# Optimization experiments

Hardware: AMD Instinct MI355X
Metric: run time of the kernel (lower is better)

## Reference

```python
import jax, jax.numpy as jnp
import numpy as np

BS, TPD, D = 16384, 4, 128
G, M = 4, 4096


def setup_inputs() -> dict:
    key = jax.random.key(0)
    k1, k2 = jax.random.split(key)
    return {
        "x": jax.random.normal(k1, (BS, TPD, D), dtype=jnp.float32),
        "embeddings": jax.random.normal(k2, (G, M, D), dtype=jnp.float32),
        "count": jnp.zeros((G, M), dtype=jnp.float32),
    }


def reference(x, embeddings, count):
    bs, tpd, d = x.shape
    g, m, _ = embeddings.shape
    # (BS, TPD, D) -> (N, G, D) -> (G, N, D), N = BS*TPD/G
    xg = x.reshape(-1, g, d).transpose(1, 0, 2)
    # squared euclidean distances (argmin identical to cdist argmin)
    x2 = jnp.sum(xg * xg, axis=-1)[:, :, None]            # (G, N, 1)
    e2 = jnp.sum(embeddings * embeddings, axis=-1)[:, None, :]  # (G, 1, M)
    dist = x2 + e2 - 2.0 * jnp.einsum('gnd,gmd->gnm', xg, embeddings)  # (G, N, M)
    indices = jnp.argmin(dist, axis=-1)                   # (G, N) int
    # usage-count scatter add (buffer update in torch forward)
    new_count = count.at[jnp.arange(g)[:, None], indices].add(1.0)
    # gather quantized embeddings: (G, N, D)
    x_quant = embeddings[jnp.arange(g)[:, None], indices]
    x_quant = x_quant.transpose(1, 0, 2).reshape(bs, tpd, d)
    ind_out = indices.transpose(1, 0).reshape(bs, tpd)
    return (x_quant, ind_out, new_count)
```

## Files before the change

kernel.cpp:

```cpp
#include <hip/hip_runtime.h>

#define G 4
#define M 4096
#define D 128
#define NQ 16384
#define NROWS 65536
#define OFF_IND 8388608
#define OFF_CNT (OFF_IND + NROWS)
#define DELTA 0.02f

typedef unsigned int u32;
typedef unsigned short u16;
typedef __attribute__((ext_vector_type(8))) short bf16x8;
typedef __attribute__((ext_vector_type(4))) float f32x4;
typedef __attribute__((ext_vector_type(16))) float f32x16;

__device__ __forceinline__ u16 f2bf(float f) {
    u32 u = __float_as_uint(f);
    return (u16)((u + 0x7FFFu + ((u >> 16) & 1u)) >> 16);
}
__device__ __forceinline__ float bf2f(u16 b) { return __uint_as_float((u32)b << 16); }

union bfpack { bf16x8 v; u32 u[4]; };


__global__ __launch_bounds__(256) void e2both(const float* __restrict__ emb,
                                              float* __restrict__ e2f,
                                              double* __restrict__ e2d,
                                              int* __restrict__ flagcnt) {
    const int row = blockIdx.x * 4 + (threadIdx.x >> 6);
    const int lane = threadIdx.x & 63;
    const float2 v = ((const float2*)(emb + (size_t)row * D))[lane];
    double s = (double)v.x * (double)v.x + (double)v.y * (double)v.y;
#pragma unroll
    for (int off = 1; off < 64; off <<= 1) s += __shfl_xor(s, off, 64);
    if (lane == 0) { e2f[row] = (float)s; e2d[row] = s; }
    if (blockIdx.x == 0 && threadIdx.x == 0) *flagcnt = 0;
}

__global__ __launch_bounds__(256) void prep_emb(const float* __restrict__ emb,
                                                u32* __restrict__ efrag) {
    const int tid = threadIdx.x;
    const int g = blockIdx.x >> 7, mt = blockIdx.x & 127;
    u32* chunk = efrag + (size_t)(g * 128 + mt) * 4096;
#pragma unroll
    for (int rep = 0; rep < 2; ++rep) {
        const int idx = rep * 256 + tid;
        const int kk = idx >> 6, lane = idx & 63;
        const int m = mt * 32 + (lane & 31);
        const int k = kk * 16 + (lane >> 5) * 8;
        const float* src = emb + ((size_t)g * M + m) * D + k;
        const float4 a = *(const float4*)src;
        const float4 b = *(const float4*)(src + 4);
        const float v[8] = {a.x, a.y, a.z, a.w, b.x, b.y, b.z, b.w};
        u32 hi[4], lo[4];
#pragma unroll
        for (int i = 0; i < 4; ++i) {
            const float v0 = v[2 * i], v1 = v[2 * i + 1];
            const u16 h0 = f2bf(v0), h1 = f2bf(v1);
            const u16 l0 = f2bf(v0 - bf2f(h0)), l1 = f2bf(v1 - bf2f(h1));
            hi[i] = (u32)h0 | ((u32)h1 << 16);
            lo[i] = (u32)l0 | ((u32)l1 << 16);
        }
        *(uint4*)(chunk + (size_t)((kk * 2 + 0) * 64 + lane) * 4) = make_uint4(hi[0], hi[1], hi[2], hi[3]);
        *(uint4*)(chunk + (size_t)((kk * 2 + 1) * 64 + lane) * 4) = make_uint4(lo[0], lo[1], lo[2], lo[3]);
    }
}

__global__ __launch_bounds__(256, 3) void vq_mfma3(const float* __restrict__ x,
                                                   const u32* __restrict__ efrag,
                                                   const float* __restrict__ e2f,
                                                   float* __restrict__ pb1,
                                                   float* __restrict__ pb2,
                                                   int* __restrict__ pi1) {
    __shared__ float e2s[2048];
    __shared__ u32 ebuf[2][4096];

    const int tid = threadIdx.x, w = tid >> 6, lane = tid & 63;
    const int combo = blockIdx.x & 7;
    const int g = combo >> 1, half = combo & 1;
    const int qb = blockIdx.x >> 3;

    const float* e2g = e2f + (size_t)g * M + half * 2048;
    for (int i = tid; i < 512; i += 256) ((float4*)e2s)[i] = ((const float4*)e2g)[i];

    const int qrow = qb * 128 + w * 32 + (lane & 31);
    bf16x8 xh[8], xl[8];
#pragma unroll
    for (int kk = 0; kk < 8; ++kk) {
        const int k = kk * 16 + (lane >> 5) * 8;
        const float* src = x + ((size_t)qrow * 4 + g) * D + k;
        const float4 a = *(const float4*)src;
        const float4 b = *(const float4*)(src + 4);
        const float v[8] = {a.x, a.y, a.z, a.w, b.x, b.y, b.z, b.w};
        bfpack ph, pl;
#pragma unroll
        for (int i = 0; i < 4; ++i) {
            const float v0 = -2.0f * v[2 * i], v1 = -2.0f * v[2 * i + 1];
            const u16 h0 = f2bf(v0), h1 = f2bf(v1);
            const u16 l0 = f2bf(v0 - bf2f(h0)), l1 = f2bf(v1 - bf2f(h1));
            ph.u[i] = (u32)h0 | ((u32)h1 << 16);
            pl.u[i] = (u32)l0 | ((u32)l1 << 16);
        }
        xh[kk] = ph.v;
        xl[kk] = pl.v;
    }

    float b1[16], b2[16];
    int i1[16];
#pragma unroll
    for (int r = 0; r < 16; ++r) { b1[r] = 3.4e38f; b2[r] = 3.4e38f; i1[r] = 0; }

    const uint4* eg = (const uint4*)(efrag + (size_t)(g * 128 + half * 64) * 4096);
    {
        const uint4 t0 = eg[tid], t1 = eg[256 + tid], t2 = eg[512 + tid], t3 = eg[768 + tid];
        uint4* db = (uint4*)ebuf[0];
        db[tid] = t0; db[256 + tid] = t1; db[512 + tid] = t2; db[768 + tid] = t3;
    }
    __syncthreads();

    for (int t = 0; t < 64; ++t) {
        const int cur = t & 1;
        uint4 s0, s1, s2, s3;
        if (t < 63) {
            const uint4* src = eg + (size_t)(t + 1) * 1024;
            s0 = src[tid]; s1 = src[256 + tid]; s2 = src[512 + tid]; s3 = src[768 + tid];
        }
        const bf16x8* bp = (const bf16x8*)ebuf[cur];
        const float e2c = e2s[t * 32 + (lane & 31)];
        f32x16 acc;
#pragma unroll
        for (int r = 0; r < 16; ++r) acc[r] = e2c;
        __builtin_amdgcn_s_setprio(1);
#pragma unroll
        for (int kk = 0; kk < 8; ++kk) {
            const bf16x8 bh = bp[(kk * 2 + 0) * 64 + lane];
            const bf16x8 bl = bp[(kk * 2 + 1) * 64 + lane];
            acc = __builtin_amdgcn_mfma_f32_32x32x16_bf16(xl[kk], bh, acc, 0, 0, 0);
            acc = __builtin_amdgcn_mfma_f32_32x32x16_bf16(xh[kk], bl, acc, 0, 0, 0);
            acc = __builtin_amdgcn_mfma_f32_32x32x16_bf16(xh[kk], bh, acc, 0, 0, 0);
        }
        __builtin_amdgcn_s_setprio(0);
        const int mcol = half * 2048 + t * 32 + (lane & 31);
#pragma unroll
        for (int r = 0; r < 16; ++r) {
            const float s = acc[r];
            b2[r] = __builtin_amdgcn_fmed3f(s, b1[r], b2[r]);
            i1[r] = (s < b1[r]) ? mcol : i1[r];
            b1[r] = fminf(b1[r], s);
        }
        if (t < 63) {
            uint4* db = (uint4*)ebuf[cur ^ 1];
            db[tid] = s0; db[256 + tid] = s1; db[512 + tid] = s2; db[768 + tid] = s3;
        }
        __syncthreads();
    }

#pragma unroll
    for (int r = 0; r < 16; ++r) {
        float v1 = b1[r], v2 = b2[r];
        int j1 = i1[r];
#pragma unroll
        for (int off = 1; off < 32; off <<= 1) {
            const float o1 = __shfl_xor(v1, off, 64);
            const int   oj = __shfl_xor(j1, off, 64);
            const float o2 = __shfl_xor(v2, off, 64);
            v2 = fminf(fminf(v2, o2), fmaxf(v1, o1));
            if (o1 < v1 || (o1 == v1 && oj < j1)) { v1 = o1; j1 = oj; }
        }
        if ((lane & 31) == 0) {
            const int q = qb * 128 + w * 32 + (r & 3) + 8 * (r >> 2) + 4 * (lane >> 5);
            const int pidx = ((((g << 14) | q)) << 1) | half;
            pb1[pidx] = v1;
            pb2[pidx] = v2;
            pi1[pidx] = j1;
        }
    }
}

__global__ __launch_bounds__(256) void merge_kernel(const float* __restrict__ pb1,
                                                    const float* __restrict__ pb2,
                                                    const int* __restrict__ pi1,
                                                    float* __restrict__ out,
                                                    int* __restrict__ flagcnt,
                                                    int* __restrict__ flaglist) {
    const int t = blockIdx.x * 256 + threadIdx.x;
    const float v1a = pb1[2 * t], v1b = pb1[2 * t + 1];
    const float v2a = pb2[2 * t], v2b = pb2[2 * t + 1];
    const int   ia = pi1[2 * t],  ib = pi1[2 * t + 1];
    const float v1 = fminf(v1a, v1b);
    const int   i  = (v1b < v1a) ? ib : ia;
    const float v2 = fminf(fminf(v2a, v2b), fmaxf(v1a, v1b));
    const int g = t >> 14, n = t & 16383;
    if (v2 - v1 > DELTA) {
        out[(size_t)OFF_IND + (size_t)n * 4 + g] = (float)i;
        atomicAdd(out + OFF_CNT + (size_t)g * M + i, 1.0f);
    } else {
        const int pos = atomicAdd(flagcnt, 1);
        flaglist[pos] = t;
    }
}

__global__ __launch_bounds__(256) void recheck(const float* __restrict__ x,
                                               const float* __restrict__ emb,
                                               const double* __restrict__ e2d,
                                               const int* __restrict__ flagcnt,
                                               const int* __restrict__ flaglist,
                                               float* __restrict__ out) {
    __shared__ float xs[D];
    __shared__ double wv[4];
    __shared__ int wi[4];
    const int tid = threadIdx.x;
    int nf = *flagcnt;
    if (nf > NROWS) nf = NROWS;
    for (int it = blockIdx.x; it < nf; it += gridDim.x) {
        const int qid = flaglist[it];
        const int g = qid >> 14, n = qid & 16383;
        __syncthreads();
        if (tid < 32) ((float4*)xs)[tid] = ((const float4*)(x + ((size_t)n * 4 + g) * D))[tid];
        __syncthreads();
        double best = 1e300;
        int bi = 0;
        for (int j = 0; j < 16; ++j) {
            const int m = tid + j * 256;
            const float* e = emb + ((size_t)g * M + m) * D;
            double dot = 0.0;
            for (int k = 0; k < D; k += 4) {
                const float4 ev = *(const float4*)(e + k);
                dot = fma((double)xs[k + 0], (double)ev.x, dot);
                dot = fma((double)xs[k + 1], (double)ev.y, dot);
                dot = fma((double)xs[k + 2], (double)ev.z, dot);
                dot = fma((double)xs[k + 3], (double)ev.w, dot);
            }
            const double s = e2d[(size_t)g * M + m] - 2.0 * dot;
            if (s < best) { best = s; bi = m; }
        }
        for (int off = 1; off < 64; off <<= 1) {
            const double ob = __shfl_xor(best, off, 64);
            const int oi = __shfl_xor(bi, off, 64);
            if (ob < best || (ob == best && oi < bi)) { best = ob; bi = oi; }
        }
        if ((tid & 63) == 0) { wv[tid >> 6] = best; wi[tid >> 6] = bi; }
        __syncthreads();
        if (tid == 0) {
            double bv = wv[0];
            int bj = wi[0];
            for (int u = 1; u < 4; ++u)
                if (wv[u] < bv || (wv[u] == bv && wi[u] < bj)) { bv = wv[u]; bj = wi[u]; }
            out[(size_t)OFF_IND + (size_t)n * 4 + g] = (float)bj;
            atomicAdd(out + OFF_CNT + (size_t)g * M + bj, 1.0f);
        }
    }
}

__global__ __launch_bounds__(256) void gather_kernel(const float* __restrict__ emb,
                                                     const float* __restrict__ indf,
                                                     float* __restrict__ xq) {
    const int rid = blockIdx.x * 8 + (threadIdx.x >> 5);
    const int lane = threadIdx.x & 31;
    const int g = rid & 3;
    const int m = (int)indf[rid];
    const float4 v = ((const float4*)(emb + ((size_t)g * M + m) * D))[lane];
    ((float4*)(xq + (size_t)rid * D))[lane] = v;
}


#define QT 64
#define MT 128
#define KT 32
#define XPAD 132
#define EPAD 36

__global__ __launch_bounds__(256) void e2d_kernel(const float* __restrict__ emb,
                                                  double* __restrict__ e2) {
    int row = blockIdx.x * 4 + (threadIdx.x >> 6);
    int lane = threadIdx.x & 63;
    const float2 v = ((const float2*)(emb + (size_t)row * D))[lane];
    double s = (double)v.x * (double)v.x + (double)v.y * (double)v.y;
#pragma unroll
    for (int off = 1; off < 64; off <<= 1) s += __shfl_xor(s, off, 64);
    if (lane == 0) e2[row] = s;
}

__global__ __launch_bounds__(256) void argmin_kernel(const float* __restrict__ x,
                                                     const float* __restrict__ emb,
                                                     const double* __restrict__ e2,
                                                     float* __restrict__ out) {
    __shared__ float xs[QT][XPAD];
    __shared__ float es[MT][EPAD];
    const int g = blockIdx.x >> 8;
    const int n0 = (blockIdx.x & 255) * QT;
    const int tid = threadIdx.x;
    const int tm = tid & 15;
    const int tq = tid >> 4;
#pragma unroll
    for (int it = 0; it < 8; ++it) {
        int idx = it * 256 + tid;
        int r = idx >> 5, c2 = idx & 31;
        const float4 v = ((const float4*)(x + ((size_t)((n0 + r) * 4 + g)) * D))[c2];
        *(float4*)&xs[r][c2 * 4] = v;
    }
    double best[4];
    int bm[4];
#pragma unroll
    for (int qi = 0; qi < 4; ++qi) { best[qi] = 1e300; bm[qi] = 0; }
    const double* e2g = e2 + (size_t)g * M;
    const float* eg = emb + (size_t)g * M * D;
    for (int mc = 0; mc < M / MT; ++mc) {
        const int m0 = mc * MT;
        double acc[4][8];
#pragma unroll
        for (int qi = 0; qi < 4; ++qi)
#pragma unroll
            for (int mi = 0; mi < 8; ++mi) acc[qi][mi] = 0.0;
        for (int kc = 0; kc < D / KT; ++kc) {
            __syncthreads();
#pragma unroll
            for (int it = 0; it < 4; ++it) {
                int idx = it * 256 + tid;
                int r = idx >> 3, c2 = idx & 7;
                const float4 v = ((const float4*)(eg + (size_t)(m0 + r) * D + kc * KT))[c2];
                *(float4*)&es[r][c2 * 4] = v;
            }
            __syncthreads();
#pragma unroll
            for (int kk = 0; kk < KT; kk += 4) {
                double xv[4][4];
#pragma unroll
                for (int qi = 0; qi < 4; ++qi) {
                    const float4 v = *(const float4*)&xs[tq + 16 * qi][kc * KT + kk];
                    xv[qi][0] = v.x; xv[qi][1] = v.y; xv[qi][2] = v.z; xv[qi][3] = v.w;
                }
#pragma unroll
                for (int mi = 0; mi < 8; ++mi) {
                    const float4 v = *(const float4*)&es[tm + 16 * mi][kk];
                    const double e0 = v.x, e1 = v.y, e2v = v.z, e3 = v.w;
#pragma unroll
                    for (int qi = 0; qi < 4; ++qi) {
                        acc[qi][mi] = fma(xv[qi][0], e0, acc[qi][mi]);
                        acc[qi][mi] = fma(xv[qi][1], e1, acc[qi][mi]);
                        acc[qi][mi] = fma(xv[qi][2], e2v, acc[qi][mi]);
                        acc[qi][mi] = fma(xv[qi][3], e3, acc[qi][mi]);
                    }
                }
            }
        }
#pragma unroll
        for (int mi = 0; mi < 8; ++mi) {
            const int m = m0 + tm + 16 * mi;
            const double e2m = e2g[m];
#pragma unroll
            for (int qi = 0; qi < 4; ++qi) {
                const double s = e2m - 2.0 * acc[qi][mi];
                if (s < best[qi]) { best[qi] = s; bm[qi] = m; }
            }
        }
    }
#pragma unroll
    for (int qi = 0; qi < 4; ++qi) {
        double v = best[qi];
        int i = bm[qi];
#pragma unroll
        for (int off = 1; off < 16; off <<= 1) {
            const double ov = __shfl_xor(v, off, 64);
            const int oi = __shfl_xor(i, off, 64);
            if (ov < v || (ov == v && oi < i)) { v = ov; i = oi; }
        }
        if (tm == 0) {
            const int n = n0 + tq + 16 * qi;
            out[(size_t)OFF_IND + (size_t)n * 4 + g] = (float)i;
            atomicAdd(out + OFF_CNT + (size_t)g * M + i, 1.0f);
        }
    }
}


extern "C" void kernel_launch(void* const* d_in, const int* in_sizes, int n_in,
                              void* d_out, int out_size, void* d_ws, size_t ws_size,
                              hipStream_t stream) {
    const float* x   = (const float*)d_in[0];
    const float* emb = (const float*)d_in[1];
    const float* cnt = (const float*)d_in[2];
    float* out = (float*)d_out;

    if (ws_size >= 8454148) {
        u32*    efrag   = (u32*)d_ws;
        float*  e2fp    = (float*)((char*)d_ws + 8388608);
        int*    flagcnt = (int*)((char*)d_ws + 8454144);
        float*  pb1      = out;
        float*  pb2      = out + 131072;
        int*    pi1      = (int*)(out + 262144);
        int*    flaglist = (int*)(out + 393216);
        double* e2d      = (double*)(out + 458752);

        hipLaunchKernelGGL(e2both, dim3(4096), dim3(256), 0, stream, emb, e2fp, e2d, flagcnt);
        hipLaunchKernelGGL(prep_emb, dim3(512), dim3(256), 0, stream, emb, efrag);
        hipMemcpyAsync(out + OFF_CNT, cnt, (size_t)G * M * sizeof(float),
                       hipMemcpyDeviceToDevice, stream);
        hipLaunchKernelGGL(vq_mfma3, dim3(1024), dim3(256), 0, stream,
                           x, efrag, e2fp, pb1, pb2, pi1);
        hipLaunchKernelGGL(merge_kernel, dim3(256), dim3(256), 0, stream,
                           pb1, pb2, pi1, out, flagcnt, flaglist);
        hipLaunchKernelGGL(recheck, dim3(2048), dim3(256), 0, stream,
                           x, emb, e2d, flagcnt, flaglist, out);
        hipLaunchKernelGGL(gather_kernel, dim3(NROWS / 8), dim3(256), 0, stream,
                           emb, out + OFF_IND, out);
    } else {
        double* e2 = (double*)d_ws;
        hipLaunchKernelGGL(e2d_kernel, dim3(4096), dim3(256), 0, stream, emb, e2);
        hipMemcpyAsync(out + OFF_CNT, cnt, (size_t)G * M * sizeof(float),
                       hipMemcpyDeviceToDevice, stream);
        hipLaunchKernelGGL(argmin_kernel, dim3((NQ / QT) * G), dim3(256), 0, stream,
                           x, emb, e2, out);
        hipLaunchKernelGGL(gather_kernel, dim3(NROWS / 8), dim3(256), 0, stream,
                           emb, out + OFF_IND, out);
    }
}
```

Baseline: 375.2 us.

## Fuse prep kernels, use direct LDS loads, merge gather into argmin merge

```diff
diff --git a/kernel.cpp b/kernel.cpp
--- a/kernel.cpp
+++ b/kernel.cpp
@@ -23,26 +23,23 @@
 
 union bfpack { bf16x8 v; u32 u[4]; };
 
-
-__global__ __launch_bounds__(256) void e2both(const float* __restrict__ emb,
-                                              float* __restrict__ e2f,
-                                              double* __restrict__ e2d,
-                                              int* __restrict__ flagcnt) {
-    const int row = blockIdx.x * 4 + (threadIdx.x >> 6);
-    const int lane = threadIdx.x & 63;
-    const float2 v = ((const float2*)(emb + (size_t)row * D))[lane];
-    double s = (double)v.x * (double)v.x + (double)v.y * (double)v.y;
-#pragma unroll
-    for (int off = 1; off < 64; off <<= 1) s += __shfl_xor(s, off, 64);
-    if (lane == 0) { e2f[row] = (float)s; e2d[row] = s; }
-    if (blockIdx.x == 0 && threadIdx.x == 0) *flagcnt = 0;
-}
-
-__global__ __launch_bounds__(256) void prep_emb(const float* __restrict__ emb,
-                                                u32* __restrict__ efrag) {
-    const int tid = threadIdx.x;
+__device__ __forceinline__ void gload16(const void* gsrc, void* ldsdst) {
+    __builtin_amdgcn_global_load_lds(
+        (const __attribute__((address_space(1))) u32*)gsrc,
+        (__attribute__((address_space(3))) u32*)ldsdst,
+        16, 0, 0);
+}
+
+
+__global__ __launch_bounds__(256) void prep_all(const float* __restrict__ emb,
+                                                u32* __restrict__ efrag,
+                                                float* __restrict__ e2f,
+                                                int* __restrict__ flagcnt) {
+    __shared__ float part[4][32];
+    const int tid = threadIdx.x, w = tid >> 6;
     const int g = blockIdx.x >> 7, mt = blockIdx.x & 127;
     u32* chunk = efrag + (size_t)(g * 128 + mt) * 4096;
+    float ss = 0.f;
 #pragma unroll
     for (int rep = 0; rep < 2; ++rep) {
         const int idx = rep * 256 + tid;
@@ -53,6 +50,8 @@
         const float4 a = *(const float4*)src;
         const float4 b = *(const float4*)(src + 4);
         const float v[8] = {a.x, a.y, a.z, a.w, b.x, b.y, b.z, b.w};
+#pragma unroll
+        for (int i = 0; i < 8; ++i) ss = fmaf(v[i], v[i], ss);
         u32 hi[4], lo[4];
 #pragma unroll
         for (int i = 0; i < 4; ++i) {
@@ -65,14 +64,18 @@
         *(uint4*)(chunk + (size_t)((kk * 2 + 0) * 64 + lane) * 4) = make_uint4(hi[0], hi[1], hi[2], hi[3]);
         *(uint4*)(chunk + (size_t)((kk * 2 + 1) * 64 + lane) * 4) = make_uint4(lo[0], lo[1], lo[2], lo[3]);
     }
-}
-
-__global__ __launch_bounds__(256, 3) void vq_mfma3(const float* __restrict__ x,
+    ss += __shfl_xor(ss, 32, 64);
+    if ((tid & 63) < 32) part[w][tid & 31] = ss;
+    __syncthreads();
+    if (tid < 32)
+        e2f[(size_t)g * M + mt * 32 + tid] = part[0][tid] + part[1][tid] + part[2][tid] + part[3][tid];
+    if (blockIdx.x == 0 && tid == 0) *flagcnt = 0;
+}
+
+__global__ __launch_bounds__(256, 3) void vq_mfma4(const float* __restrict__ x,
                                                    const u32* __restrict__ efrag,
                                                    const float* __restrict__ e2f,
-                                                   float* __restrict__ pb1,
-                                                   float* __restrict__ pb2,
-                                                   int* __restrict__ pi1) {
+                                                   float* __restrict__ out) {
     __shared__ float e2s[2048];
     __shared__ u32 ebuf[2][4096];
 
@@ -111,27 +114,27 @@
 #pragma unroll
     for (int r = 0; r < 16; ++r) { b1[r] = 3.4e38f; b2[r] = 3.4e38f; i1[r] = 0; }
 
-    const uint4* eg = (const uint4*)(efrag + (size_t)(g * 128 + half * 64) * 4096);
-    {
-        const uint4 t0 = eg[tid], t1 = eg[256 + tid], t2 = eg[512 + tid], t3 = eg[768 + tid];
-        uint4* db = (uint4*)ebuf[0];
-        db[tid] = t0; db[256 + tid] = t1; db[512 + tid] = t2; db[768 + tid] = t3;
-    }
+    const char* eg = (const char*)(efrag + (size_t)(g * 128 + half * 64) * 4096);
+#pragma unroll
+    for (int j = 0; j < 4; ++j)
+        gload16(eg + j * 4096 + w * 1024 + lane * 16,
+                (char*)ebuf[0] + j * 4096 + w * 1024);
     __syncthreads();
 
+    int cur = 0;
     for (int t = 0; t < 64; ++t) {
-        const int cur = t & 1;
-        uint4 s0, s1, s2, s3;
         if (t < 63) {
-            const uint4* src = eg + (size_t)(t + 1) * 1024;
-            s0 = src[tid]; s1 = src[256 + tid]; s2 = src[512 + tid]; s3 = src[768 + tid];
+            const char* src = eg + (size_t)(t + 1) * 16384;
+#pragma unroll
+            for (int j = 0; j < 4; ++j)
+                gload16(src + j * 4096 + w * 1024 + lane * 16,
+                        (char*)ebuf[cur ^ 1] + j * 4096 + w * 1024);
         }
         const bf16x8* bp = (const bf16x8*)ebuf[cur];
         const float e2c = e2s[t * 32 + (lane & 31)];
         f32x16 acc;
 #pragma unroll
         for (int r = 0; r < 16; ++r) acc[r] = e2c;
-        __builtin_amdgcn_s_setprio(1);
 #pragma unroll
         for (int kk = 0; kk < 8; ++kk) {
             const bf16x8 bh = bp[(kk * 2 + 0) * 64 + lane];
@@ -140,7 +143,6 @@
             acc = __builtin_amdgcn_mfma_f32_32x32x16_bf16(xh[kk], bl, acc, 0, 0, 0);
             acc = __builtin_amdgcn_mfma_f32_32x32x16_bf16(xh[kk], bh, acc, 0, 0, 0);
         }
-        __builtin_amdgcn_s_setprio(0);
         const int mcol = half * 2048 + t * 32 + (lane & 31);
 #pragma unroll
         for (int r = 0; r < 16; ++r) {
@@ -149,11 +151,8 @@
             i1[r] = (s < b1[r]) ? mcol : i1[r];
             b1[r] = fminf(b1[r], s);
         }
-        if (t < 63) {
-            uint4* db = (uint4*)ebuf[cur ^ 1];
-            db[tid] = s0; db[256 + tid] = s1; db[512 + tid] = s2; db[768 + tid] = s3;
-        }
         __syncthreads();
+        cur ^= 1;
     }
 
 #pragma unroll
@@ -170,46 +169,63 @@
         }
         if ((lane & 31) == 0) {
             const int q = qb * 128 + w * 32 + (r & 3) + 8 * (r >> 2) + 4 * (lane >> 5);
-            const int pidx = ((((g << 14) | q)) << 1) | half;
-            pb1[pidx] = v1;
-            pb2[pidx] = v2;
-            pi1[pidx] = j1;
-        }
-    }
-}
-
-__global__ __launch_bounds__(256) void merge_kernel(const float* __restrict__ pb1,
-                                                    const float* __restrict__ pb2,
-                                                    const int* __restrict__ pi1,
+            float* rowbase = out + (size_t)(q * 4 + g) * D;
+            *(float4*)(rowbase + half * 4) =
+                make_float4(v1, v2, __int_as_float(j1), 0.f);
+        }
+    }
+}
+
+__global__ __launch_bounds__(256) void gather_merge(const float* __restrict__ emb,
                                                     float* __restrict__ out,
                                                     int* __restrict__ flagcnt,
                                                     int* __restrict__ flaglist) {
-    const int t = blockIdx.x * 256 + threadIdx.x;
-    const float v1a = pb1[2 * t], v1b = pb1[2 * t + 1];
-    const float v2a = pb2[2 * t], v2b = pb2[2 * t + 1];
-    const int   ia = pi1[2 * t],  ib = pi1[2 * t + 1];
-    const float v1 = fminf(v1a, v1b);
-    const int   i  = (v1b < v1a) ? ib : ia;
-    const float v2 = fminf(fminf(v2a, v2b), fmaxf(v1a, v1b));
-    const int g = t >> 14, n = t & 16383;
-    if (v2 - v1 > DELTA) {
+    __shared__ int sm[64];
+    const int tid = threadIdx.x;
+    const int qid0 = blockIdx.x * 64;
+    const int g = qid0 >> 14;
+    if (tid < 64) {
+        const int qid = qid0 + tid;
+        const int n = qid & 16383;
+        float* rowbase = out + (size_t)(n * 4 + g) * D;
+        const float4 p0 = *(const float4*)(rowbase);
+        const float4 p1 = *(const float4*)(rowbase + 4);
+        const float v1a = p0.x, v2a = p0.y;
+        const float v1b = p1.x, v2b = p1.y;
+        const int ia = __float_as_int(p0.z), ib = __float_as_int(p1.z);
+        const float v1 = fminf(v1a, v1b);
+        const int i = (v1b < v1a) ? ib : ia;
+        const float v2 = fminf(fminf(v2a, v2b), fmaxf(v1a, v1b));
         out[(size_t)OFF_IND + (size_t)n * 4 + g] = (float)i;
-        atomicAdd(out + OFF_CNT + (size_t)g * M + i, 1.0f);
-    } else {
-        const int pos = atomicAdd(flagcnt, 1);
-        flaglist[pos] = t;
-    }
-}
-
-__global__ __launch_bounds__(256) void recheck(const float* __restrict__ x,
-                                               const float* __restrict__ emb,
-                                               const double* __restrict__ e2d,
-                                               const int* __restrict__ flagcnt,
-                                               const int* __restrict__ flaglist,
-                                               float* __restrict__ out) {
+        if (v2 - v1 > DELTA) {
+            atomicAdd(out + OFF_CNT + (size_t)g * M + i, 1.0f);
+        } else {
+            const int pos = atomicAdd(flagcnt, 1);
+            flaglist[pos] = qid;
+        }
+        sm[tid] = i;
+    }
+    __syncthreads();
+#pragma unroll
+    for (int p = 0; p < 8; ++p) {
+        const int t2 = p * 8 + (tid >> 5);
+        const int lane = tid & 31;
+        const int n = (qid0 + t2) & 16383;
+        const int m = sm[t2];
+        const float4 v = ((const float4*)(emb + ((size_t)g * M + m) * D))[lane];
+        ((float4*)(out + (size_t)(n * 4 + g) * D))[lane] = v;
+    }
+}
+
+__global__ __launch_bounds__(256) void recheck2(const float* __restrict__ x,
+                                                const float* __restrict__ emb,
+                                                const int* __restrict__ flagcnt,
+                                                const int* __restrict__ flaglist,
+                                                float* __restrict__ out) {
     __shared__ float xs[D];
     __shared__ double wv[4];
     __shared__ int wi[4];
+    __shared__ int sbj;
     const int tid = threadIdx.x;
     int nf = *flagcnt;
     if (nf > NROWS) nf = NROWS;
@@ -224,15 +240,18 @@
         for (int j = 0; j < 16; ++j) {
             const int m = tid + j * 256;
             const float* e = emb + ((size_t)g * M + m) * D;
-            double dot = 0.0;
+            double dot = 0.0, ee = 0.0;
             for (int k = 0; k < D; k += 4) {
                 const float4 ev = *(const float4*)(e + k);
-                dot = fma((double)xs[k + 0], (double)ev.x, dot);
-                dot = fma((double)xs[k + 1], (double)ev.y, dot);
-                dot = fma((double)xs[k + 2], (double)ev.z, dot);
-                dot = fma((double)xs[k + 3], (double)ev.w, dot);
+                const double e0 = ev.x, e1 = ev.y, e2v = ev.z, e3 = ev.w;
+                dot = fma((double)xs[k + 0], e0, dot);
+                dot = fma((double)xs[k + 1], e1, dot);
+                dot = fma((double)xs[k + 2], e2v, dot);
+                dot = fma((double)xs[k + 3], e3, dot);
+                ee = fma(e0, e0, ee); ee = fma(e1, e1, ee);
+                ee = fma(e2v, e2v, ee); ee = fma(e3, e3, ee);
             }
-            const double s = e2d[(size_t)g * M + m] - 2.0 * dot;
+            const double s = ee - 2.0 * dot;
             if (s < best) { best = s; bi = m; }
         }
         for (int off = 1; off < 64; off <<= 1) {
@@ -249,19 +268,15 @@
                 if (wv[u] < bv || (wv[u] == bv && wi[u] < bj)) { bv = wv[u]; bj = wi[u]; }
             out[(size_t)OFF_IND + (size_t)n * 4 + g] = (float)bj;
             atomicAdd(out + OFF_CNT + (size_t)g * M + bj, 1.0f);
-        }
-    }
-}
-
-__global__ __launch_bounds__(256) void gather_kernel(const float* __restrict__ emb,
-                                                     const float* __restrict__ indf,
-                                                     float* __restrict__ xq) {
-    const int rid = blockIdx.x * 8 + (threadIdx.x >> 5);
-    const int lane = threadIdx.x & 31;
-    const int g = rid & 3;
-    const int m = (int)indf[rid];
-    const float4 v = ((const float4*)(emb + ((size_t)g * M + m) * D))[lane];
-    ((float4*)(xq + (size_t)rid * D))[lane] = v;
+            sbj = bj;
+        }
+        __syncthreads();
+        if (tid < 32) {
+            const int bj = sbj;
+            ((float4*)(out + (size_t)(n * 4 + g) * D))[tid] =
+                ((const float4*)(emb + ((size_t)g * M + bj) * D))[tid];
+        }
+    }
 }
 
 
@@ -374,6 +389,17 @@
     }
 }
 
+__global__ __launch_bounds__(256) void gather_kernel(const float* __restrict__ emb,
+                                                     const float* __restrict__ indf,
+                                                     float* __restrict__ xq) {
+    const int rid = blockIdx.x * 8 + (threadIdx.x >> 5);
+    const int lane = threadIdx.x & 31;
+    const int g = rid & 3;
+    const int m = (int)indf[rid];
+    const float4 v = ((const float4*)(emb + ((size_t)g * M + m) * D))[lane];
+    ((float4*)(xq + (size_t)rid * D))[lane] = v;
+}
+
 
 extern "C" void kernel_launch(void* const* d_in, const int* in_sizes, int n_in,
                               void* d_out, int out_size, void* d_ws, size_t ws_size,
@@ -383,28 +409,22 @@
     const float* cnt = (const float*)d_in[2];
     float* out = (float*)d_out;
 
-    if (ws_size >= 8454148) {
-        u32*    efrag   = (u32*)d_ws;
-        float*  e2fp    = (float*)((char*)d_ws + 8388608);
-        int*    flagcnt = (int*)((char*)d_ws + 8454144);
-        float*  pb1      = out;
-        float*  pb2      = out + 131072;
-        int*    pi1      = (int*)(out + 262144);
-        int*    flaglist = (int*)(out + 393216);
-        double* e2d      = (double*)(out + 458752);
-
-        hipLaunchKernelGGL(e2both, dim3(4096), dim3(256), 0, stream, emb, e2fp, e2d, flagcnt);
-        hipLaunchKernelGGL(prep_emb, dim3(512), dim3(256), 0, stream, emb, efrag);
+    if (ws_size >= 8716544) {
+        u32*   efrag    = (u32*)d_ws;
+        float* e2fp     = (float*)((char*)d_ws + 8388608);
+        int*   flagcnt  = (int*)((char*)d_ws + 8454144);
+        int*   flaglist = (int*)((char*)d_ws + 8454400);
+
+        hipLaunchKernelGGL(prep_all, dim3(512), dim3(256), 0, stream,
+                           emb, efrag, e2fp, flagcnt);
         hipMemcpyAsync(out + OFF_CNT, cnt, (size_t)G * M * sizeof(float),
                        hipMemcpyDeviceToDevice, stream);
-        hipLaunchKernelGGL(vq_mfma3, dim3(1024), dim3(256), 0, stream,
-                           x, efrag, e2fp, pb1, pb2, pi1);
-        hipLaunchKernelGGL(merge_kernel, dim3(256), dim3(256), 0, stream,
-                           pb1, pb2, pi1, out, flagcnt, flaglist);
-        hipLaunchKernelGGL(recheck, dim3(2048), dim3(256), 0, stream,
-                           x, emb, e2d, flagcnt, flaglist, out);
-        hipLaunchKernelGGL(gather_kernel, dim3(NROWS / 8), dim3(256), 0, stream,
-                           emb, out + OFF_IND, out);
+        hipLaunchKernelGGL(vq_mfma4, dim3(1024), dim3(256), 0, stream,
+                           x, efrag, e2fp, out);
+        hipLaunchKernelGGL(gather_merge, dim3(1024), dim3(256), 0, stream,
+                           emb, out, flagcnt, flaglist);
+        hipLaunchKernelGGL(recheck2, dim3(2048), dim3(256), 0, stream,
+                           x, emb, flagcnt, flaglist, out);
     } else {
         double* e2 = (double*)d_ws;
         hipLaunchKernelGGL(e2d_kernel, dim3(4096), dim3(256), 0, stream, emb, e2);
```

New measurement: 366.3 us. 2.4% less time.
